# Kernel optimization log

Measured on AMD Instinct MI355X. Metric: run time of the kernel, lower is better.

The kernel has to match this reference:

```python
import jax, jax.numpy as jnp
import numpy as np

Dm = 512      # d_model
DI = 1024     # d_inner = 2*d_model (expand=2)
DR = 32       # dt_rank = ceil(d_model/16)
DC = 4        # d_conv
T = 3
Bb, Sf, H, W = 2, 15, 16, 11


def _ln(x, g, b):
    m = jnp.mean(x, axis=-1, keepdims=True)
    v = jnp.var(x, axis=-1, keepdims=True)
    return (x - m) * jax.lax.rsqrt(v + 1e-5) * g + b


def _mamba(x, in_w, conv_w, conv_b, xproj_w, dtproj_w, dtproj_b, A_log, D_param, out_w):
    # x: (B, L, Dm). Standard Mamba block with d_state=1.
    B, L, _ = x.shape
    xz = x @ in_w.T                                  # (B, L, 2*DI)
    xi, z = jnp.split(xz, 2, axis=-1)                # each (B, L, DI)
    # causal depthwise conv1d, kernel DC
    xc = jnp.transpose(xi, (0, 2, 1))                # (B, DI, L)
    xc = jax.lax.conv_general_dilated(
        xc, conv_w[:, None, :], (1,), [(DC - 1, 0)],
        dimension_numbers=('NCH', 'OIH', 'NCH'), feature_group_count=DI)
    xc = xc + conv_b[None, :, None]
    xi = jax.nn.silu(jnp.transpose(xc, (0, 2, 1)))   # (B, L, DI)
    x_dbl = xi @ xproj_w.T                           # (B, L, DR + 2)  (d_state=1)
    dt = x_dbl[..., :DR]
    Bc = x_dbl[..., DR:DR + 1]                       # (B, L, 1)
    Cc = x_dbl[..., DR + 1:DR + 2]                   # (B, L, 1)
    dt = jax.nn.softplus(dt @ dtproj_w.T + dtproj_b)  # (B, L, DI)
    A = -jnp.exp(A_log[:, 0])                        # (DI,), d_state=1
    dA = jnp.exp(dt * A)                             # (B, L, DI)
    dBx = dt * Bc * xi                               # (B, L, DI)
    # linear recurrence h_t = dA_t * h_{t-1} + dBx_t via parallel scan
    def comb(l, r):
        return (l[0] * r[0], r[0] * l[1] + r[1])
    _, h = jax.lax.associative_scan(comb, (dA, dBx), axis=1)
    y = Cc * h + D_param * xi                        # (B, L, DI)
    y = y * jax.nn.silu(z)
    return y @ out_w.T                               # (B, L, Dm)


def setup_inputs() -> dict:
    key = jax.random.key(0)
    ks = jax.random.split(key, 10)
    p = {}
    p['x'] = jax.random.normal(ks[0], (Bb, Sf, H, W, Dm), jnp.float32)
    p['ln1_g'] = jnp.ones((Dm,), jnp.float32)
    p['ln1_b'] = jnp.zeros((Dm,), jnp.float32)
    p['ln2_g'] = jnp.ones((Dm,), jnp.float32)
    p['ln2_b'] = jnp.zeros((Dm,), jnp.float32)
    p['mlp_w1'] = jax.random.normal(ks[1], (4 * Dm, Dm), jnp.float32) * 0.02
    p['mlp_b1'] = jnp.zeros((4 * Dm,), jnp.float32)
    p['mlp_w2'] = jax.random.normal(ks[2], (Dm, 4 * Dm), jnp.float32) * 0.02
    p['mlp_b2'] = jnp.zeros((Dm,), jnp.float32)
    p['in_w'] = jax.random.normal(ks[3], (2 * DI, Dm), jnp.float32) * 0.02
    p['conv_w'] = jax.random.normal(ks[4], (DI, DC), jnp.float32) * 0.1
    p['conv_b'] = jnp.zeros((DI,), jnp.float32)
    p['xproj_w'] = jax.random.normal(ks[5], (DR + 2, DI), jnp.float32) * 0.02
    p['dtproj_w'] = jax.random.normal(ks[6], (DI, DR), jnp.float32) * 0.1
    p['dtproj_b'] = jax.random.normal(ks[7], (DI,), jnp.float32) * 0.1
    p['A_log'] = jnp.zeros((DI, 1), jnp.float32)     # A = -1 per channel (mamba init, d_state=1)
    p['D_param'] = jnp.ones((DI,), jnp.float32)
    p['out_w'] = jax.random.normal(ks[8], (Dm, DI), jnp.float32) * 0.02
    return p


def reference(x, ln1_g, ln1_b, ln2_g, ln2_b, mlp_w1, mlp_b1, mlp_w2, mlp_b2,
              in_w, conv_w, conv_b, xproj_w, dtproj_w, dtproj_b, A_log, D_param, out_w):
    b, S, h, w, c = x.shape
    s = S // T
    xr = x.reshape(b * s, T, h, w, c)
    Bm, L = b * s, T * h * w
    # ---- part1: 4-directional mamba over flattened/flipped sequences ----
    xn = _ln(xr, ln1_g, ln1_b)
    x1 = xn.reshape(Bm, L, c)                                  # b (s h w) c
    x3 = jnp.transpose(xn, (0, 1, 3, 2, 4)).reshape(Bm, L, c)  # b (s w h) c
    cat = jnp.concatenate([x1, jnp.flip(x1, 1), x3, jnp.flip(x3, 1)], axis=0)
    y = _mamba(cat, in_w, conv_w, conv_b, xproj_w, dtproj_w, dtproj_b, A_log, D_param, out_w)
    y1, y2, y3, y4 = jnp.split(y, 4, axis=0)
    x12 = (y1 + jnp.flip(y2, 1)).reshape(Bm, T, h, w, c)
    x34 = jnp.transpose((y3 + jnp.flip(y4, 1)).reshape(Bm, T, w, h, c), (0, 1, 3, 2, 4))
    xr = xr + x12 + x34   # dropout (eval) = identity
    # ---- part2: MLP ----
    hmid = jax.nn.gelu(_ln(xr, ln2_g, ln2_b) @ mlp_w1.T + mlp_b1, approximate=False)
    xr = xr + (hmid @ mlp_w2.T + mlp_b2)
    return xr.reshape(b, S, h, w, c)
```

## Files before the change

kernel.cpp:

```cpp
#include <hip/hip_runtime.h>
#include <math.h>

typedef __attribute__((ext_vector_type(8))) short short8;
typedef __attribute__((ext_vector_type(8))) __bf16 bf16x8;
typedef __attribute__((ext_vector_type(4))) float f32x4;
typedef unsigned short ushort_t;

#define DEV __device__ __forceinline__

constexpr int Dm   = 512;
constexpr int DI   = 1024;
constexpr int DR   = 32;
constexpr int Hh   = 16;
constexpr int Wd   = 11;
constexpr int Bm   = 10;
constexpr int Lq   = 528;
constexpr int NTOK = Bm * Lq;
constexpr int MBAT = 4 * Bm;
constexpr int MTOK = MBAT * Lq;
constexpr int XD_LD = 64;
constexpr int NCHK = 16;
constexpr int CHK  = Lq / NCHK;
constexpr int MPAD = 5376;

DEV ushort_t f2bf(float f) {
    unsigned u = __float_as_uint(f);
    u += 0x7fffu + ((u >> 16) & 1u);
    return (ushort_t)(u >> 16);
}
DEV float bf2f(ushort_t h) { return __uint_as_float(((unsigned)h) << 16); }

DEV bf16x8 as_bf(short8 v) { return __builtin_bit_cast(bf16x8, v); }

DEV void mfma_bf16(f32x4& d, short8 a, short8 b) {
    d = __builtin_amdgcn_mfma_f32_16x16x32_bf16(as_bf(a), as_bf(b), d, 0, 0, 0);
}

DEV void gll16(const ushort_t* g, ushort_t* l) {
    __builtin_amdgcn_global_load_lds((const __attribute__((address_space(1))) void*)g,
                                     (__attribute__((address_space(3))) void*)l,
                                     16, 0, 0);
}

template<int N> DEV void vm_wait() {
    if constexpr (N == 0) asm volatile("s_waitcnt vmcnt(0)" ::: "memory");
    else if constexpr (N == 2) asm volatile("s_waitcnt vmcnt(2)" ::: "memory");
    else if constexpr (N == 3) asm volatile("s_waitcnt vmcnt(3)" ::: "memory");
    else if constexpr (N == 4) asm volatile("s_waitcnt vmcnt(4)" ::: "memory");
    else asm volatile("s_waitcnt vmcnt(6)" ::: "memory");
}

DEV float fast_erf(float x) {
    const float ax = fabsf(x);
    const float t  = 1.0f / (1.0f + 0.3275911f * ax);
    const float y  = t * (0.254829592f + t * (-0.284496736f + t * (1.421413741f
                   + t * (-1.453152027f + t * 1.061405429f))));
    const float r  = 1.0f - y * __expf(-ax * ax);
    return copysignf(r, x);
}

DEV int path_tok(int p, int bi, int q) {
    int ql = (p & 1) ? (Lq - 1 - q) : q;
    int l1;
    if (p < 2) {
        l1 = ql;
    } else {
        int t   = ql / (Hh * Wd);
        int rem = ql - t * (Hh * Wd);
        int ww  = rem / Hh;
        int hh  = rem - ww * Hh;
        l1 = (t * Hh + hh) * Wd + ww;
    }
    return bi * Lq + l1;
}

constexpr int PR0 = 2 * DI * Dm;
constexpr int PR1 = PR0 + Dm * DI;
constexpr int PR2 = PR1 + 4 * Dm * Dm;
constexpr int PR3 = PR2 + Dm * 4 * Dm;
constexpr int PR4 = PR3 + 64 * DI;
constexpr int PR5 = PR4 + DI * 64;
constexpr int PR6 = PR5 + 4 * DI;
__global__ void k_prep(const float* __restrict__ in_w,  const float* __restrict__ out_w,
                       const float* __restrict__ w1,    const float* __restrict__ w2,
                       const float* __restrict__ xproj, const float* __restrict__ dtproj,
                       const float* __restrict__ cw,
                       ushort_t* __restrict__ w_in,  ushort_t* __restrict__ w_out,
                       ushort_t* __restrict__ w_1,   ushort_t* __restrict__ w_2,
                       ushort_t* __restrict__ w_xp,  ushort_t* __restrict__ w_dt,
                       float* __restrict__ cwT) {
    int i = blockIdx.x * 256 + threadIdx.x;
    if (i < PR0)      { w_in [i]       = f2bf(in_w [i]); }
    else if (i < PR1) { w_out[i - PR0] = f2bf(out_w[i - PR0]); }
    else if (i < PR2) { w_1  [i - PR1] = f2bf(w1   [i - PR1]); }
    else if (i < PR3) { w_2  [i - PR2] = f2bf(w2   [i - PR2]); }
    else if (i < PR4) {
        int j = i - PR3;
        int n = j / DI, k = j - n * DI;
        w_xp[j] = (n < DR + 2) ? f2bf(xproj[n * DI + k]) : (ushort_t)0;
    } else if (i < PR5) {
        int j = i - PR4;
        int r = j >> 6, c = j & 63;
        w_dt[j] = (c < DR) ? f2bf(dtproj[r * DR + c]) : (ushort_t)0;
    } else if (i < PR6) {
        int j = i - PR5;
        int d = j / DI, ch = j - d * DI;
        cwT[j] = cw[ch * 4 + d];
    }
}

__global__ void k_ln1(const float* __restrict__ x, const float* __restrict__ g,
                      const float* __restrict__ b, ushort_t* __restrict__ xn) {
    const int tok  = blockIdx.x;
    const int lane = threadIdx.x;
    const int c0   = lane * 8;
    const float* row = x + (size_t)tok * Dm;
    float4 v0 = *(const float4*)(row + c0);
    float4 v1 = *(const float4*)(row + c0 + 4);
    float s  = v0.x + v0.y + v0.z + v0.w + v1.x + v1.y + v1.z + v1.w;
    float ss = v0.x*v0.x + v0.y*v0.y + v0.z*v0.z + v0.w*v0.w
             + v1.x*v1.x + v1.y*v1.y + v1.z*v1.z + v1.w*v1.w;
#pragma unroll
    for (int o = 32; o >= 1; o >>= 1) { s += __shfl_xor(s, o); ss += __shfl_xor(ss, o); }
    const float mean = s * (1.0f / Dm);
    const float rstd = rsqrtf(ss * (1.0f / Dm) - mean * mean + 1e-5f);
    float4 g0 = *(const float4*)(g + c0), g1 = *(const float4*)(g + c0 + 4);
    float4 b0 = *(const float4*)(b + c0), b1 = *(const float4*)(b + c0 + 4);
    union { uint4 u; ushort_t h[8]; } pk;
    pk.h[0] = f2bf((v0.x - mean) * rstd * g0.x + b0.x);
    pk.h[1] = f2bf((v0.y - mean) * rstd * g0.y + b0.y);
    pk.h[2] = f2bf((v0.z - mean) * rstd * g0.z + b0.z);
    pk.h[3] = f2bf((v0.w - mean) * rstd * g0.w + b0.w);
    pk.h[4] = f2bf((v1.x - mean) * rstd * g1.x + b1.x);
    pk.h[5] = f2bf((v1.y - mean) * rstd * g1.y + b1.y);
    pk.h[6] = f2bf((v1.z - mean) * rstd * g1.z + b1.z);
    pk.h[7] = f2bf((v1.w - mean) * rstd * g1.w + b1.w);
    *(uint4*)(xn + (size_t)tok * Dm + c0) = pk.u;
}

template<int BM, int BN, int EPI>
__launch_bounds__(512)
__global__ void k_gemm8w(const ushort_t* __restrict__ A, const ushort_t* __restrict__ B,
                         void* __restrict__ C, int M, int K,
                         int lda, int ldb, int ldc, int nst,
                         const float* __restrict__ bias, const float* __restrict__ resid) {
    constexpr int FM = BM / 32;
    constexpr int FN = BN / 64;
    constexpr int AP = BM / 64;
    constexpr int BP = BN / 64;
    constexpr int LPS = AP + BP;
    __shared__ __align__(16) ushort_t As[2][BM * 64];
    __shared__ __align__(16) ushort_t Bs[2][BN * 64];
    const int tid  = threadIdx.x;
    const int lane = tid & 63;
    const int w    = tid >> 6;
    const int wm   = w >> 2, wn = w & 3;
    const int lr   = lane & 15, lg = lane >> 4;
    const int m0   = blockIdx.x * BM, n0 = blockIdx.y * BN;

    f32x4 acc[FM][FN] = {};

    auto stage = [&](int buf, int kb) {
#pragma unroll
        for (int i = 0; i < AP; ++i) {
            const int chunk = i * 512 + tid;
            const int r    = chunk >> 3;
            const int ccol = chunk & 7;
            const int csrc = ccol ^ (r & 7);
            gll16(A + (size_t)(m0 + r) * lda + kb + csrc * 8, As[buf] + chunk * 8);
        }
#pragma unroll
        for (int i = 0; i < BP; ++i) {
            const int chunk = i * 512 + tid;
            const int r    = chunk >> 3;
            const int ccol = chunk & 7;
            const int csrc = ccol ^ (r & 7);
            gll16(B + (size_t)(n0 + r) * ldb + kb + csrc * 8, Bs[buf] + chunk * 8);
        }
    };

    auto compute = [&](int buf) {
#pragma unroll
        for (int kk = 0; kk < 2; ++kk) {
            short8 a[FM], b[FN];
#pragma unroll
            for (int mf = 0; mf < FM; ++mf) {
                const int row = wm * (BM / 2) + mf * 16 + lr;
                const int pc  = (kk * 4 + lg) ^ (row & 7);
                a[mf] = *(const short8*)(As[buf] + (size_t)row * 64 + pc * 8);
            }
#pragma unroll
            for (int nf = 0; nf < FN; ++nf) {
                const int row = wn * (BN / 4) + nf * 16 + lr;
                const int pc  = (kk * 4 + lg) ^ (row & 7);
                b[nf] = *(const short8*)(Bs[buf] + (size_t)row * 64 + pc * 8);
            }
#pragma unroll
            for (int mf = 0; mf < FM; ++mf)
#pragma unroll
                for (int nf = 0; nf < FN; ++nf)
                    mfma_bf16(acc[mf][nf], a[mf], b[nf]);
        }
    };

    const int nt = K >> 6;
    stage(0, 0);
    if (nt > 1) stage(1, 64);
    for (int t = 0; t < nt; ++t) {
        if (t + 1 < nt) vm_wait<LPS>();
        else            vm_wait<0>();
        __builtin_amdgcn_s_barrier();
        compute(t & 1);
        if (t + 2 < nt) {
            __builtin_amdgcn_s_barrier();
            stage(t & 1, (t + 2) << 6);
        }
    }

#pragma unroll
    for (int mf = 0; mf < FM; ++mf)
#pragma unroll
        for (int nf = 0; nf < FN; ++nf) {
            const int gc = n0 + wn * (BN / 4) + nf * 16 + lr;
            if (gc >= nst) continue;
#pragma unroll
            for (int r = 0; r < 4; ++r) {
                const int gm = m0 + wm * (BM / 2) + mf * 16 + lg * 4 + r;
                if (gm >= M) continue;
                float v = acc[mf][nf][r];
                const size_t oi = (size_t)gm * ldc + gc;
                if constexpr (EPI == 0) {
                    ((ushort_t*)C)[oi] = f2bf(v);
                } else if constexpr (EPI == 1) {
                    v += bias[gc];
                    v = fmaxf(v, 0.0f) + __logf(1.0f + __expf(-fabsf(v)));
                    ((ushort_t*)C)[oi] = f2bf(v);
                } else if constexpr (EPI == 2) {
                    v += bias[gc];
                    v = 0.5f * v * (1.0f + fast_erf(v * 0.70710678118654752f));
                    ((ushort_t*)C)[oi] = f2bf(v);
                } else if constexpr (EPI == 3) {
                    v += bias[gc] + resid[oi];
                    ((float*)C)[oi] = v;
                } else if constexpr (EPI == 4) {
                    v += resid[oi];
                    ((float*)C)[oi] = v;
                }
            }
        }
}

__global__ void k_conv(const ushort_t* __restrict__ xz0, const float* __restrict__ cwT,
                       const float* __restrict__ cb, ushort_t* __restrict__ xi) {
    const int idx = blockIdx.x * 256 + threadIdx.x;
    if (idx >= MTOK * 128) return;
    const int g  = idx & 127;
    const int c0 = g * 8;
    const int l  = (idx >> 7) % Lq;
    const int s  = idx / (128 * Lq);
    const int p  = s / Bm, bi = s % Bm;
    float a[8];
    {
        float4 b0 = *(const float4*)(cb + c0);
        float4 b1 = *(const float4*)(cb + c0 + 4);
        a[0]=b0.x; a[1]=b0.y; a[2]=b0.z; a[3]=b0.w;
        a[4]=b1.x; a[5]=b1.y; a[6]=b1.z; a[7]=b1.w;
    }
#pragma unroll
    for (int d = 0; d < 4; ++d) {
        const int lq = l - (3 - d);
        if (lq < 0) continue;
        const int tok = path_tok(p, bi, lq);
        union U { uint4 u; ushort_t h[8]; } xv;
        xv.u = *(const uint4*)(xz0 + (size_t)tok * (2 * DI) + c0);
        const float4 w0 = *(const float4*)(cwT + d * DI + c0);
        const float4 w1 = *(const float4*)(cwT + d * DI + c0 + 4);
        a[0] += bf2f(xv.h[0]) * w0.x;
        a[1] += bf2f(xv.h[1]) * w0.y;
        a[2] += bf2f(xv.h[2]) * w0.z;
        a[3] += bf2f(xv.h[3]) * w0.w;
        a[4] += bf2f(xv.h[4]) * w1.x;
        a[5] += bf2f(xv.h[5]) * w1.y;
        a[6] += bf2f(xv.h[6]) * w1.z;
        a[7] += bf2f(xv.h[7]) * w1.w;
    }
    union U { uint4 u; ushort_t h[8]; } ov;
#pragma unroll
    for (int k = 0; k < 8; ++k) {
        const float sv = a[k] / (1.0f + __expf(-a[k]));
        ov.h[k] = f2bf(sv);
    }
    *(uint4*)(xi + (size_t)(s * Lq + l) * DI + c0) = ov.u;
}

__global__ void k_scan1(const ushort_t* __restrict__ dt,
                        const ushort_t* __restrict__ xdbl, const float* __restrict__ A_log,
                        const float* __restrict__ Dp, ushort_t* __restrict__ xiy,
                        ushort_t* __restrict__ corr, float* __restrict__ Pb,
                        float* __restrict__ Sb) {
    const int blk = blockIdx.x;
    const int cg = blk & 15;
    const int j  = (blk >> 4) & (NCHK - 1);
    const int s  = blk >> 8;
    const int ch = (cg << 6) + threadIdx.x;
    const int gl0 = j * CHK;
    const float Av = -__expf(A_log[ch]);
    const float Dv = Dp[ch];
    const size_t tok0 = (size_t)s * Lq + (size_t)gl0;
    const ushort_t* pdt = dt  + tok0 * DI + ch;
    ushort_t*       pxi = xiy + tok0 * DI + ch;
    ushort_t*       pco = corr + tok0 * DI + ch;
    const ushort_t* pbc = xdbl + tok0 * XD_LD;

    float h = 0.0f, pp = 1.0f;
    float dtv = bf2f(pdt[0]);
    float xiv = bf2f(pxi[0]);
    float bc  = bf2f(pbc[32]);
    float cc  = bf2f(pbc[33]);
    for (int l = 0; l < CHK; ++l) {
        float ndt = 0.f, nxi = 0.f, nbc = 0.f, ncc = 0.f;
        if (l + 1 < CHK) {
            const size_t o = (size_t)(l + 1);
            ndt = bf2f(pdt[o * DI]);
            nxi = bf2f(pxi[o * DI]);
            nbc = bf2f(pbc[o * XD_LD + 32]);
            ncc = bf2f(pbc[o * XD_LD + 33]);
        }
        const float dA = __expf(dtv * Av);
        h = dA * h + dtv * bc * xiv;
        pp *= dA;
        pxi[(size_t)l * DI] = f2bf(cc * h + Dv * xiv);
        pco[(size_t)l * DI] = f2bf(cc * pp);
        dtv = ndt; xiv = nxi; bc = nbc; cc = ncc;
    }
    const size_t pi = (size_t)(s * NCHK + j) * DI + ch;
    Pb[pi] = pp;
    Sb[pi] = h;
}

__global__ void k_scan2(const float* __restrict__ Pb, const float* __restrict__ Sb,
                        float* __restrict__ cb) {
    const int s  = blockIdx.x >> 4;
    const int ch = ((blockIdx.x & 15) << 6) + threadIdx.x;
    float c = 0.0f;
#pragma unroll
    for (int j = 0; j < NCHK; ++j) {
        const size_t pi = (size_t)(s * NCHK + j) * DI + ch;
        cb[pi] = c;
        c = Pb[pi] * c + Sb[pi];
    }
}

__global__ void k_ysum(const ushort_t* __restrict__ y, const ushort_t* __restrict__ corr,
                       const float* __restrict__ cbuf, const ushort_t* __restrict__ xz0,
                       ushort_t* __restrict__ ys) {
    const int tok = blockIdx.x;
    const int c0  = threadIdx.x * 8;
    const int bi = tok / Lq;
    const int l1 = tok % Lq;
    const int t  = l1 / (Hh * Wd);
    const int hw = l1 % (Hh * Wd);
    const int hh = hw / Wd, ww = hw % Wd;
    const int l3 = (t * Wd + ww) * Hh + hh;
    const int q[4] = { l1, Lq - 1 - l1, l3, Lq - 1 - l3 };
    float a[8] = {};
#pragma unroll
    for (int p = 0; p < 4; ++p) {
        const int sq = p * Bm + bi;
        const size_t off = ((size_t)sq * Lq + q[p]) * DI + c0;
        union U { uint4 u; ushort_t h[8]; } yv, cv;
        yv.u = *(const uint4*)(y + off);
        cv.u = *(const uint4*)(corr + off);
        const int j = q[p] / CHK;
        const float* cp = cbuf + ((size_t)sq * NCHK + j) * DI + c0;
        float4 ca = *(const float4*)(cp);
        float4 cb2 = *(const float4*)(cp + 4);
        a[0] += bf2f(yv.h[0]) + ca.x  * bf2f(cv.h[0]);
        a[1] += bf2f(yv.h[1]) + ca.y  * bf2f(cv.h[1]);
        a[2] += bf2f(yv.h[2]) + ca.z  * bf2f(cv.h[2]);
        a[3] += bf2f(yv.h[3]) + ca.w  * bf2f(cv.h[3]);
        a[4] += bf2f(yv.h[4]) + cb2.x * bf2f(cv.h[4]);
        a[5] += bf2f(yv.h[5]) + cb2.y * bf2f(cv.h[5]);
        a[6] += bf2f(yv.h[6]) + cb2.z * bf2f(cv.h[6]);
        a[7] += bf2f(yv.h[7]) + cb2.w * bf2f(cv.h[7]);
    }
    union Z { uint4 u; ushort_t h[8]; } zv;
    zv.u = *(const uint4*)(xz0 + (size_t)tok * (2 * DI) + DI + c0);
    union U { uint4 u; ushort_t h[8]; } ov;
#pragma unroll
    for (int k = 0; k < 8; ++k) {
        const float z = bf2f(zv.h[k]);
        ov.h[k] = f2bf(a[k] * z / (1.0f + __expf(-z)));
    }
    *(uint4*)(ys + (size_t)tok * DI + c0) = ov.u;
}

__global__ void k_ln2(const float* __restrict__ xin, const float* __restrict__ g,
                      const float* __restrict__ b, ushort_t* __restrict__ out) {
    const int tok  = blockIdx.x;
    const int lane = threadIdx.x;
    const int c0   = lane * 8;
    const float* row = xin + (size_t)tok * Dm;
    float4 v0 = *(const float4*)(row + c0);
    float4 v1 = *(const float4*)(row + c0 + 4);
    float s  = v0.x + v0.y + v0.z + v0.w + v1.x + v1.y + v1.z + v1.w;
    float ss = v0.x*v0.x + v0.y*v0.y + v0.z*v0.z + v0.w*v0.w
             + v1.x*v1.x + v1.y*v1.y + v1.z*v1.z + v1.w*v1.w;
#pragma unroll
    for (int o = 32; o >= 1; o >>= 1) { s += __shfl_xor(s, o); ss += __shfl_xor(ss, o); }
    const float mean = s * (1.0f / Dm);
    const float rstd = rsqrtf(ss * (1.0f / Dm) - mean * mean + 1e-5f);
    float4 g0 = *(const float4*)(g + c0), g1 = *(const float4*)(g + c0 + 4);
    float4 b0 = *(const float4*)(b + c0), b1 = *(const float4*)(b + c0 + 4);
    union { uint4 u; ushort_t h[8]; } pk;
    pk.h[0] = f2bf((v0.x - mean) * rstd * g0.x + b0.x);
    pk.h[1] = f2bf((v0.y - mean) * rstd * g0.y + b0.y);
    pk.h[2] = f2bf((v0.z - mean) * rstd * g0.z + b0.z);
    pk.h[3] = f2bf((v0.w - mean) * rstd * g0.w + b0.w);
    pk.h[4] = f2bf((v1.x - mean) * rstd * g1.x + b1.x);
    pk.h[5] = f2bf((v1.y - mean) * rstd * g1.y + b1.y);
    pk.h[6] = f2bf((v1.z - mean) * rstd * g1.z + b1.z);
    pk.h[7] = f2bf((v1.w - mean) * rstd * g1.w + b1.w);
    *(uint4*)(out + (size_t)tok * Dm + c0) = pk.u;
}

constexpr size_t OFF_CAT = 0;
constexpr size_t SZ_CAT  = (size_t)MPAD * Dm * 2;
constexpr size_t OFF_XZ0 = OFF_CAT + SZ_CAT;
constexpr size_t SZ_XZ0  = (size_t)MPAD * 2 * DI * 2;
constexpr size_t OFF_XI  = OFF_XZ0 + SZ_XZ0;
constexpr size_t SZ_XI   = (size_t)MTOK * DI * 2;
constexpr size_t OFF_XD  = OFF_XI + SZ_XI;
constexpr size_t SZ_XD   = (size_t)MTOK * XD_LD * 2;
constexpr size_t OFF_DT  = OFF_XD + SZ_XD;
constexpr size_t SZ_DT   = (size_t)MTOK * DI * 2;
constexpr size_t OFF_CO  = OFF_DT + SZ_DT;
constexpr size_t SZ_CO   = (size_t)MTOK * DI * 2;
constexpr size_t SZ_PSC  = (size_t)MBAT * NCHK * DI * 4;
constexpr size_t OFF_P   = OFF_CO + SZ_CO;
constexpr size_t OFF_S   = OFF_P + SZ_PSC;
constexpr size_t OFF_C   = OFF_S + SZ_PSC;
constexpr size_t OFF_YS  = OFF_C + SZ_PSC;
constexpr size_t SZ_YS   = (size_t)MPAD * DI * 2;
constexpr size_t OFF_XR2 = OFF_YS + SZ_YS;
constexpr size_t SZ_XR2  = (size_t)NTOK * Dm * 4;
constexpr size_t OFF_XL2 = OFF_XR2 + SZ_XR2;
constexpr size_t SZ_XL2  = (size_t)MPAD * Dm * 2;
constexpr size_t OFF_HM  = OFF_XL2 + SZ_XL2;
constexpr size_t SZ_HM   = (size_t)MPAD * 4 * Dm * 2;
constexpr size_t OFF_WIN = OFF_HM + SZ_HM;
constexpr size_t OFF_WOUT= OFF_WIN  + (size_t)2 * DI * Dm * 2;
constexpr size_t OFF_W1  = OFF_WOUT + (size_t)Dm * DI * 2;
constexpr size_t OFF_W2  = OFF_W1   + (size_t)4 * Dm * Dm * 2;
constexpr size_t OFF_WXP = OFF_W2   + (size_t)Dm * 4 * Dm * 2;
constexpr size_t OFF_WDT = OFF_WXP  + (size_t)64 * DI * 2;
constexpr size_t OFF_CWT = OFF_WDT  + (size_t)DI * 64 * 2;
constexpr size_t WS_NEED = OFF_CWT  + (size_t)4 * DI * 4;

extern "C" void kernel_launch(void* const* d_in, const int* in_sizes, int n_in,
                              void* d_out, int out_size, void* d_ws, size_t ws_size,
                              hipStream_t stream) {
    const float* x        = (const float*)d_in[0];
    const float* ln1_g    = (const float*)d_in[1];
    const float* ln1_b    = (const float*)d_in[2];
    const float* ln2_g    = (const float*)d_in[3];
    const float* ln2_b    = (const float*)d_in[4];
    const float* mlp_w1   = (const float*)d_in[5];
    const float* mlp_b1   = (const float*)d_in[6];
    const float* mlp_w2   = (const float*)d_in[7];
    const float* mlp_b2   = (const float*)d_in[8];
    const float* in_w     = (const float*)d_in[9];
    const float* conv_w   = (const float*)d_in[10];
    const float* conv_b   = (const float*)d_in[11];
    const float* xproj_w  = (const float*)d_in[12];
    const float* dtproj_w = (const float*)d_in[13];
    const float* dtproj_b = (const float*)d_in[14];
    const float* A_log    = (const float*)d_in[15];
    const float* D_param  = (const float*)d_in[16];
    const float* out_w    = (const float*)d_in[17];

    if (ws_size < WS_NEED) return;

    char* ws = (char*)d_ws;
    ushort_t* cat   = (ushort_t*)(ws + OFF_CAT);
    ushort_t* xz0   = (ushort_t*)(ws + OFF_XZ0);
    ushort_t* xi    = (ushort_t*)(ws + OFF_XI);
    ushort_t* xdbl  = (ushort_t*)(ws + OFF_XD);
    ushort_t* dtb   = (ushort_t*)(ws + OFF_DT);
    ushort_t* corr  = (ushort_t*)(ws + OFF_CO);
    float*    Pb    = (float*)   (ws + OFF_P);
    float*    Sb    = (float*)   (ws + OFF_S);
    float*    cb    = (float*)   (ws + OFF_C);
    ushort_t* ysum  = (ushort_t*)(ws + OFF_YS);
    float*    xr2   = (float*)   (ws + OFF_XR2);
    ushort_t* xln2  = (ushort_t*)(ws + OFF_XL2);
    ushort_t* hmid  = (ushort_t*)(ws + OFF_HM);
    ushort_t* w_in  = (ushort_t*)(ws + OFF_WIN);
    ushort_t* w_out = (ushort_t*)(ws + OFF_WOUT);
    ushort_t* w_1   = (ushort_t*)(ws + OFF_W1);
    ushort_t* w_2   = (ushort_t*)(ws + OFF_W2);
    ushort_t* w_xp  = (ushort_t*)(ws + OFF_WXP);
    ushort_t* w_dt  = (ushort_t*)(ws + OFF_WDT);
    float*    cwT   = (float*)   (ws + OFF_CWT);

    k_prep<<<(PR6 + 255) / 256, 256, 0, stream>>>(
        in_w, out_w, mlp_w1, mlp_w2, xproj_w, dtproj_w, conv_w,
        w_in, w_out, w_1, w_2, w_xp, w_dt, cwT);

    k_ln1<<<NTOK, 64, 0, stream>>>(x, ln1_g, ln1_b, cat);

    k_gemm8w<64, 128, 0><<<dim3(MPAD / 64, (2 * DI) / 128), 512, 0, stream>>>(
        cat, w_in, xz0, NTOK, Dm, Dm, Dm, 2 * DI, 2 * DI, nullptr, nullptr);

    k_conv<<<(MTOK * 128 + 255) / 256, 256, 0, stream>>>(xz0, cwT, conv_b, xi);

    k_gemm8w<64, 64, 0><<<dim3(MTOK / 64, 1), 512, 0, stream>>>(
        xi, w_xp, xdbl, MTOK, DI, DI, DI, XD_LD, 64, nullptr, nullptr);

    k_gemm8w<64, 128, 1><<<dim3(MTOK / 64, DI / 128), 512, 0, stream>>>(
        xdbl, w_dt, dtb, MTOK, 64, XD_LD, 64, DI, DI, dtproj_b, nullptr);

    k_scan1<<<MBAT * NCHK * 16, 64, 0, stream>>>(dtb, xdbl, A_log, D_param,
                                                 xi, corr, Pb, Sb);
    k_scan2<<<MBAT * 16, 64, 0, stream>>>(Pb, Sb, cb);

    k_ysum<<<NTOK, 128, 0, stream>>>(xi, corr, cb, xz0, ysum);

    k_gemm8w<64, 128, 4><<<dim3(MPAD / 64, Dm / 128), 512, 0, stream>>>(
        ysum, w_out, xr2, NTOK, DI, DI, DI, Dm, Dm, nullptr, x);

    k_ln2<<<NTOK, 64, 0, stream>>>(xr2, ln2_g, ln2_b, xln2);

    k_gemm8w<64, 128, 2><<<dim3(MPAD / 64, (4 * Dm) / 128), 512, 0, stream>>>(
        xln2, w_1, hmid, NTOK, Dm, Dm, Dm, 4 * Dm, 4 * Dm, mlp_b1, nullptr);

    k_gemm8w<64, 128, 3><<<dim3(MPAD / 64, Dm / 128), 512, 0, stream>>>(
        hmid, w_2, (float*)d_out, NTOK, 4 * Dm, 4 * Dm, 4 * Dm, Dm, Dm, mlp_b2, xr2);
}
```

Measured before the change: 241.5 us.

## Fuse dt projection and softplus into the scan kernel, dropping the dt GEMM

```diff
diff --git a/kernel.cpp b/kernel.cpp
--- a/kernel.cpp
+++ b/kernel.cpp
@@ -79,16 +79,13 @@
 constexpr int PR2 = PR1 + 4 * Dm * Dm;
 constexpr int PR3 = PR2 + Dm * 4 * Dm;
 constexpr int PR4 = PR3 + 64 * DI;
-constexpr int PR5 = PR4 + DI * 64;
-constexpr int PR6 = PR5 + 4 * DI;
+constexpr int PR5 = PR4 + 4 * DI;
 __global__ void k_prep(const float* __restrict__ in_w,  const float* __restrict__ out_w,
                        const float* __restrict__ w1,    const float* __restrict__ w2,
-                       const float* __restrict__ xproj, const float* __restrict__ dtproj,
-                       const float* __restrict__ cw,
+                       const float* __restrict__ xproj, const float* __restrict__ cw,
                        ushort_t* __restrict__ w_in,  ushort_t* __restrict__ w_out,
                        ushort_t* __restrict__ w_1,   ushort_t* __restrict__ w_2,
-                       ushort_t* __restrict__ w_xp,  ushort_t* __restrict__ w_dt,
-                       float* __restrict__ cwT) {
+                       ushort_t* __restrict__ w_xp,  float* __restrict__ cwT) {
     int i = blockIdx.x * 256 + threadIdx.x;
     if (i < PR0)      { w_in [i]       = f2bf(in_w [i]); }
     else if (i < PR1) { w_out[i - PR0] = f2bf(out_w[i - PR0]); }
@@ -100,10 +97,6 @@
         w_xp[j] = (n < DR + 2) ? f2bf(xproj[n * DI + k]) : (ushort_t)0;
     } else if (i < PR5) {
         int j = i - PR4;
-        int r = j >> 6, c = j & 63;
-        w_dt[j] = (c < DR) ? f2bf(dtproj[r * DR + c]) : (ushort_t)0;
-    } else if (i < PR6) {
-        int j = i - PR5;
         int d = j / DI, ch = j - d * DI;
         cwT[j] = cw[ch * 4 + d];
     }
@@ -231,10 +224,6 @@
                 const size_t oi = (size_t)gm * ldc + gc;
                 if constexpr (EPI == 0) {
                     ((ushort_t*)C)[oi] = f2bf(v);
-                } else if constexpr (EPI == 1) {
-                    v += bias[gc];
-                    v = fmaxf(v, 0.0f) + __logf(1.0f + __expf(-fabsf(v)));
-                    ((ushort_t*)C)[oi] = f2bf(v);
                 } else if constexpr (EPI == 2) {
                     v += bias[gc];
                     v = 0.5f * v * (1.0f + fast_erf(v * 0.70710678118654752f));
@@ -293,8 +282,8 @@
     *(uint4*)(xi + (size_t)(s * Lq + l) * DI + c0) = ov.u;
 }
 
-__global__ void k_scan1(const ushort_t* __restrict__ dt,
-                        const ushort_t* __restrict__ xdbl, const float* __restrict__ A_log,
+__global__ void k_scan1(const ushort_t* __restrict__ xdbl, const float* __restrict__ dtw,
+                        const float* __restrict__ dtbias, const float* __restrict__ A_log,
                         const float* __restrict__ Dp, ushort_t* __restrict__ xiy,
                         ushort_t* __restrict__ corr, float* __restrict__ Pb,
                         float* __restrict__ Sb) {
@@ -306,32 +295,45 @@
     const int gl0 = j * CHK;
     const float Av = -__expf(A_log[ch]);
     const float Dv = Dp[ch];
+    const float bia = dtbias[ch];
+    float wdt[32];
+#pragma unroll
+    for (int r = 0; r < 8; ++r) {
+        float4 v = *(const float4*)(dtw + (size_t)ch * DR + r * 4);
+        wdt[r*4+0] = v.x; wdt[r*4+1] = v.y; wdt[r*4+2] = v.z; wdt[r*4+3] = v.w;
+    }
     const size_t tok0 = (size_t)s * Lq + (size_t)gl0;
-    const ushort_t* pdt = dt  + tok0 * DI + ch;
     ushort_t*       pxi = xiy + tok0 * DI + ch;
     ushort_t*       pco = corr + tok0 * DI + ch;
     const ushort_t* pbc = xdbl + tok0 * XD_LD;
 
     float h = 0.0f, pp = 1.0f;
-    float dtv = bf2f(pdt[0]);
-    float xiv = bf2f(pxi[0]);
-    float bc  = bf2f(pbc[32]);
-    float cc  = bf2f(pbc[33]);
     for (int l = 0; l < CHK; ++l) {
-        float ndt = 0.f, nxi = 0.f, nbc = 0.f, ncc = 0.f;
-        if (l + 1 < CHK) {
-            const size_t o = (size_t)(l + 1);
-            ndt = bf2f(pdt[o * DI]);
-            nxi = bf2f(pxi[o * DI]);
-            nbc = bf2f(pbc[o * XD_LD + 32]);
-            ncc = bf2f(pbc[o * XD_LD + 33]);
-        }
+        const ushort_t* prow = pbc + (size_t)l * XD_LD;
+        union U { uint4 u; ushort_t h[8]; } x0, x1, x2, x3, bc2;
+        x0.u  = *(const uint4*)(prow);
+        x1.u  = *(const uint4*)(prow + 8);
+        x2.u  = *(const uint4*)(prow + 16);
+        x3.u  = *(const uint4*)(prow + 24);
+        bc2.u = *(const uint4*)(prow + 32);
+        float acc = bia;
+#pragma unroll
+        for (int r = 0; r < 8; ++r) acc += bf2f(x0.h[r]) * wdt[r];
+#pragma unroll
+        for (int r = 0; r < 8; ++r) acc += bf2f(x1.h[r]) * wdt[8 + r];
+#pragma unroll
+        for (int r = 0; r < 8; ++r) acc += bf2f(x2.h[r]) * wdt[16 + r];
+#pragma unroll
+        for (int r = 0; r < 8; ++r) acc += bf2f(x3.h[r]) * wdt[24 + r];
+        const float dtv = fmaxf(acc, 0.0f) + __logf(1.0f + __expf(-fabsf(acc)));
+        const float xiv = bf2f(pxi[(size_t)l * DI]);
+        const float bc  = bf2f(bc2.h[0]);
+        const float cc  = bf2f(bc2.h[1]);
         const float dA = __expf(dtv * Av);
         h = dA * h + dtv * bc * xiv;
         pp *= dA;
         pxi[(size_t)l * DI] = f2bf(cc * h + Dv * xiv);
         pco[(size_t)l * DI] = f2bf(cc * pp);
-        dtv = ndt; xiv = nxi; bc = nbc; cc = ncc;
     }
     const size_t pi = (size_t)(s * NCHK + j) * DI + ch;
     Pb[pi] = pp;
@@ -432,9 +434,7 @@
 constexpr size_t SZ_XI   = (size_t)MTOK * DI * 2;
 constexpr size_t OFF_XD  = OFF_XI + SZ_XI;
 constexpr size_t SZ_XD   = (size_t)MTOK * XD_LD * 2;
-constexpr size_t OFF_DT  = OFF_XD + SZ_XD;
-constexpr size_t SZ_DT   = (size_t)MTOK * DI * 2;
-constexpr size_t OFF_CO  = OFF_DT + SZ_DT;
+constexpr size_t OFF_CO  = OFF_XD + SZ_XD;
 constexpr size_t SZ_CO   = (size_t)MTOK * DI * 2;
 constexpr size_t SZ_PSC  = (size_t)MBAT * NCHK * DI * 4;
 constexpr size_t OFF_P   = OFF_CO + SZ_CO;
@@ -453,8 +453,7 @@
 constexpr size_t OFF_W1  = OFF_WOUT + (size_t)Dm * DI * 2;
 constexpr size_t OFF_W2  = OFF_W1   + (size_t)4 * Dm * Dm * 2;
 constexpr size_t OFF_WXP = OFF_W2   + (size_t)Dm * 4 * Dm * 2;
-constexpr size_t OFF_WDT = OFF_WXP  + (size_t)64 * DI * 2;
-constexpr size_t OFF_CWT = OFF_WDT  + (size_t)DI * 64 * 2;
+constexpr size_t OFF_CWT = OFF_WXP  + (size_t)64 * DI * 2;
 constexpr size_t WS_NEED = OFF_CWT  + (size_t)4 * DI * 4;
 
 extern "C" void kernel_launch(void* const* d_in, const int* in_sizes, int n_in,
@@ -486,7 +485,6 @@
     ushort_t* xz0   = (ushort_t*)(ws + OFF_XZ0);
     ushort_t* xi    = (ushort_t*)(ws + OFF_XI);
     ushort_t* xdbl  = (ushort_t*)(ws + OFF_XD);
-    ushort_t* dtb   = (ushort_t*)(ws + OFF_DT);
     ushort_t* corr  = (ushort_t*)(ws + OFF_CO);
     float*    Pb    = (float*)   (ws + OFF_P);
     float*    Sb    = (float*)   (ws + OFF_S);
@@ -500,12 +498,11 @@
     ushort_t* w_1   = (ushort_t*)(ws + OFF_W1);
     ushort_t* w_2   = (ushort_t*)(ws + OFF_W2);
     ushort_t* w_xp  = (ushort_t*)(ws + OFF_WXP);
-    ushort_t* w_dt  = (ushort_t*)(ws + OFF_WDT);
     float*    cwT   = (float*)   (ws + OFF_CWT);
 
-    k_prep<<<(PR6 + 255) / 256, 256, 0, stream>>>(
-        in_w, out_w, mlp_w1, mlp_w2, xproj_w, dtproj_w, conv_w,
-        w_in, w_out, w_1, w_2, w_xp, w_dt, cwT);
+    k_prep<<<(PR5 + 255) / 256, 256, 0, stream>>>(
+        in_w, out_w, mlp_w1, mlp_w2, xproj_w, conv_w,
+        w_in, w_out, w_1, w_2, w_xp, cwT);
 
     k_ln1<<<NTOK, 64, 0, stream>>>(x, ln1_g, ln1_b, cat);
 
@@ -517,11 +514,8 @@
     k_gemm8w<64, 64, 0><<<dim3(MTOK / 64, 1), 512, 0, stream>>>(
         xi, w_xp, xdbl, MTOK, DI, DI, DI, XD_LD, 64, nullptr, nullptr);
 
-    k_gemm8w<64, 128, 1><<<dim3(MTOK / 64, DI / 128), 512, 0, stream>>>(
-        xdbl, w_dt, dtb, MTOK, 64, XD_LD, 64, DI, DI, dtproj_b, nullptr);
-
-    k_scan1<<<MBAT * NCHK * 16, 64, 0, stream>>>(dtb, xdbl, A_log, D_param,
-                                                 xi, corr, Pb, Sb);
+    k_scan1<<<MBAT * NCHK * 16, 64, 0, stream>>>(xdbl, dtproj_w, dtproj_b,
+                                                 A_log, D_param, xi, corr, Pb, Sb);
     k_scan2<<<MBAT * 16, 64, 0, stream>>>(Pb, Sb, cb);
 
     k_ysum<<<NTOK, 128, 0, stream>>>(xi, corr, cb, xz0, ysum);
```

New measurement: 246.4 us. 2.0% more time.
